# Kernel optimization log

Hardware: AMD Instinct MI355X
Metric: run time of the kernel (lower is better)

Reference implementation:

```python
import jax, jax.numpy as jnp
import numpy as np

H = 1024
V = 50257
L = 4096

def setup_inputs() -> dict:
    key = jax.random.key(0)
    ks = jax.random.split(key, 10)
    s = 1.0 / np.sqrt(H)
    return {
        "input": jax.random.randint(ks[0], (1,), 0, V, dtype=jnp.int64),
        "hidden": jax.random.normal(ks[1], (1, 1, H), dtype=jnp.float32),
        "encoder_hiddens": jax.random.normal(ks[2], (L, H), dtype=jnp.float32),
        "embedding": jax.random.normal(ks[3], (V, H), dtype=jnp.float32),
        "w_ih": jax.random.uniform(ks[4], (3 * H, H), minval=-s, maxval=s, dtype=jnp.float32),
        "w_hh": jax.random.uniform(ks[5], (3 * H, H), minval=-s, maxval=s, dtype=jnp.float32),
        "b_ih": jax.random.uniform(ks[6], (3 * H,), minval=-s, maxval=s, dtype=jnp.float32),
        "b_hh": jax.random.uniform(ks[7], (3 * H,), minval=-s, maxval=s, dtype=jnp.float32),
        "out_w": jax.random.uniform(ks[8], (V, 2 * H), minval=-s, maxval=s, dtype=jnp.float32),
        "out_b": jax.random.uniform(ks[9], (V,), minval=-s, maxval=s, dtype=jnp.float32),
    }


def _gru_step(x, h, w_ih, w_hh, b_ih, b_hh):
    # x, h: (H,). PyTorch GRU cell gate math (gate order: r, z, n).
    gi = w_ih @ x + b_ih                      # (3H,)
    gh = w_hh @ h + b_hh                      # (3H,)
    i_r, i_z, i_n = gi[:H], gi[H:2 * H], gi[2 * H:]
    h_r, h_z, h_n = gh[:H], gh[H:2 * H], gh[2 * H:]
    r = jax.nn.sigmoid(i_r + h_r)
    z = jax.nn.sigmoid(i_z + h_z)
    n = jnp.tanh(i_n + r * h_n)
    return (1.0 - z) * n + z * h


def reference(input, hidden, encoder_hiddens, embedding, w_ih, w_hh, b_ih, b_hh, out_w, out_b):
    # Embedding lookup of single token -> (H,); dropout is identity at inference.
    x = embedding[input].reshape(-1)
    h = hidden[0, 0]                          # (H,)
    h_new = _gru_step(x, h, w_ih, w_hh, b_ih, b_hh)  # (H,)
    # Dot-product attention over encoder hiddens (L, H)
    scores = encoder_hiddens @ h_new          # (L,)
    attn = jax.nn.softmax(scores)             # (L,)
    ctx = attn @ encoder_hiddens              # (H,)
    concat = jnp.concatenate([ctx, h_new])    # (2H,)
    logits = out_w @ concat + out_b           # (V,)
    output = jax.nn.log_softmax(logits)[None, :]  # (1, V)
    return output, h_new[None, None, :]
```

## Files before the change

### kernel.cpp

```cpp
#include <hip/hip_runtime.h>
#include <hip/hip_bf16.h>

#define H 1024
#define V 50257
#define L 4096

__device__ __forceinline__ float sigmoidf_(float x) { return 1.f / (1.f + expf(-x)); }

__device__ __forceinline__ float dot4(float4 w, float4 c) {
    return w.x * c.x + w.y * c.y + w.z * c.z + w.w * c.w;
}

__global__ __launch_bounds__(64) void k_gru(const int* __restrict__ idx,
        const float* __restrict__ hidden, const float* __restrict__ emb,
        const float* __restrict__ w_ih, const float* __restrict__ w_hh,
        const float* __restrict__ b_ih, const float* __restrict__ b_hh,
        float* __restrict__ concat, float* __restrict__ out_h) {
    const int j = blockIdx.x;
    const int lane = threadIdx.x;
    const float* x   = emb + (size_t)idx[0] * H;
    const float* wir = w_ih + (size_t)j * H;
    const float* wiz = wir + (size_t)H * H;
    const float* win = wiz + (size_t)H * H;
    const float* whr = w_hh + (size_t)j * H;
    const float* whz = whr + (size_t)H * H;
    const float* whn = whz + (size_t)H * H;
    float sir = 0, siz = 0, sin_ = 0, shr = 0, shz = 0, shn = 0;
    #pragma unroll
    for (int it = 0; it < 4; ++it) {
        int elem = (it * 64 + lane) * 4;
        float4 xf = *(const float4*)(x + elem);
        float4 hf = *(const float4*)(hidden + elem);
        sir  += dot4(*(const float4*)(wir + elem), xf);
        siz  += dot4(*(const float4*)(wiz + elem), xf);
        sin_ += dot4(*(const float4*)(win + elem), xf);
        shr  += dot4(*(const float4*)(whr + elem), hf);
        shz  += dot4(*(const float4*)(whz + elem), hf);
        shn  += dot4(*(const float4*)(whn + elem), hf);
    }
    #pragma unroll
    for (int off = 32; off; off >>= 1) {
        sir += __shfl_xor(sir, off); siz += __shfl_xor(siz, off);
        sin_ += __shfl_xor(sin_, off); shr += __shfl_xor(shr, off);
        shz += __shfl_xor(shz, off); shn += __shfl_xor(shn, off);
    }
    if (lane == 0) {
        float r = sigmoidf_(sir + b_ih[j]       + shr + b_hh[j]);
        float z = sigmoidf_(siz + b_ih[H + j]   + shz + b_hh[H + j]);
        float n = tanhf(sin_ + b_ih[2*H + j] + r * (shn + b_hh[2*H + j]));
        float hn = (1.f - z) * n + z * hidden[j];
        concat[H + j] = hn;
        out_h[j] = hn;
    }
}

__global__ __launch_bounds__(256) void k_scores(const float* __restrict__ enc,
        const float* __restrict__ concat, float* __restrict__ scores) {
    const int wave = threadIdx.x >> 6, lane = threadIdx.x & 63;
    const int l = blockIdx.x * 4 + wave;
    const float* row = enc + (size_t)l * H;
    const float* h = concat + H;
    float s = 0.f;
    #pragma unroll
    for (int it = 0; it < 4; ++it) {
        int elem = (it * 64 + lane) * 4;
        s += dot4(*(const float4*)(row + elem), *(const float4*)(h + elem));
    }
    #pragma unroll
    for (int off = 32; off; off >>= 1) s += __shfl_xor(s, off);
    if (lane == 0) scores[l] = s;
}

__global__ __launch_bounds__(256) void k_softmax(const float* __restrict__ scores,
                                                 float* __restrict__ attn) {
    __shared__ float sm[8];
    const int t = threadIdx.x, lane = t & 63, wave = t >> 6;
    float v[16];
    float m = -INFINITY;
    #pragma unroll
    for (int i = 0; i < 16; ++i) { v[i] = scores[i * 256 + t]; m = fmaxf(m, v[i]); }
    #pragma unroll
    for (int off = 32; off; off >>= 1) m = fmaxf(m, __shfl_xor(m, off));
    if (lane == 0) sm[wave] = m;
    __syncthreads();
    m = fmaxf(fmaxf(sm[0], sm[1]), fmaxf(sm[2], sm[3]));
    float s = 0.f;
    #pragma unroll
    for (int i = 0; i < 16; ++i) { v[i] = expf(v[i] - m); s += v[i]; }
    #pragma unroll
    for (int off = 32; off; off >>= 1) s += __shfl_xor(s, off);
    __syncthreads();
    if (lane == 0) sm[wave] = s;
    __syncthreads();
    s = sm[0] + sm[1] + sm[2] + sm[3];
    float inv = 1.f / s;
    #pragma unroll
    for (int i = 0; i < 16; ++i) attn[i * 256 + t] = v[i] * inv;
}

__global__ __launch_bounds__(256) void k_ctx_partial(const float* __restrict__ enc,
        const float* __restrict__ attn, float* __restrict__ partial) {
    __shared__ float a[256];
    const int t = threadIdx.x;
    const int r0 = blockIdx.x * 256;
    a[t] = attn[r0 + t];
    __syncthreads();
    float acc0 = 0, acc1 = 0, acc2 = 0, acc3 = 0;
    const float* p = enc + (size_t)r0 * H + t * 4;
    for (int l = 0; l < 256; ++l) {
        float4 w = *(const float4*)p; p += H;
        float al = a[l];
        acc0 += al * w.x; acc1 += al * w.y; acc2 += al * w.z; acc3 += al * w.w;
    }
    *(float4*)(partial + (size_t)blockIdx.x * H + t * 4) = make_float4(acc0, acc1, acc2, acc3);
}

__global__ __launch_bounds__(256) void k_ctx_reduce(const float* __restrict__ partial,
                                                    float* __restrict__ concat) {
    const int c = blockIdx.x * 256 + threadIdx.x;
    float s = 0.f;
    #pragma unroll
    for (int p = 0; p < 16; ++p) s += partial[p * H + c];
    concat[c] = s;
}

__global__ __launch_bounds__(256) void k_logits(const float* __restrict__ out_w,
        const float* __restrict__ out_b, const float* __restrict__ concat,
        float* __restrict__ logits) {
    const int wave = threadIdx.x >> 6, lane = threadIdx.x & 63;
    const int v = blockIdx.x * 4 + wave;
    if (v >= V) return;
    const float* row = out_w + (size_t)v * (2 * H);
    float s = 0.f;
    #pragma unroll
    for (int it = 0; it < 8; ++it) {
        int elem = (it * 64 + lane) * 4;
        s += dot4(*(const float4*)(row + elem), *(const float4*)(concat + elem));
    }
    #pragma unroll
    for (int off = 32; off; off >>= 1) s += __shfl_xor(s, off);
    if (lane == 0) logits[v] = s + out_b[v];
}

__global__ __launch_bounds__(256) void k_lse_partial(const float* __restrict__ logits,
                                                     float* __restrict__ red) {
    __shared__ float sm[4], ss[4];
    const int t = threadIdx.x;
    const int i = blockIdx.x * 256 + t;
    float m = -INFINITY, s = 0.f;
    for (int v = i; v < V; v += 64 * 256) {
        float x = logits[v];
        float M = fmaxf(m, x);
        s = s * expf(m - M) + expf(x - M);
        m = M;
    }
    const int lane = t & 63, wave = t >> 6;
    #pragma unroll
    for (int off = 32; off; off >>= 1) {
        float m2 = __shfl_xor(m, off), s2 = __shfl_xor(s, off);
        float M = fmaxf(m, m2);
        s = s * expf(m - M) + s2 * expf(m2 - M);
        m = M;
    }
    if (lane == 0) { sm[wave] = m; ss[wave] = s; }
    __syncthreads();
    if (t == 0) {
        float M = fmaxf(fmaxf(sm[0], sm[1]), fmaxf(sm[2], sm[3]));
        float S = ss[0] * expf(sm[0] - M) + ss[1] * expf(sm[1] - M) +
                  ss[2] * expf(sm[2] - M) + ss[3] * expf(sm[3] - M);
        red[blockIdx.x] = M;
        red[64 + blockIdx.x] = S;
    }
}

__global__ __launch_bounds__(64) void k_lse_final(const float* __restrict__ red,
                                                  float* __restrict__ C) {
    const int lane = threadIdx.x;
    float m = red[lane], s = red[64 + lane];
    #pragma unroll
    for (int off = 32; off; off >>= 1) {
        float m2 = __shfl_xor(m, off), s2 = __shfl_xor(s, off);
        float M = fmaxf(m, m2);
        s = s * expf(m - M) + s2 * expf(m2 - M);
        m = M;
    }
    if (lane == 0) C[0] = m + logf(s);
}

__global__ __launch_bounds__(256) void k_write(const float* __restrict__ logits,
        const float* __restrict__ C, float* __restrict__ out) {
    const int v = blockIdx.x * 256 + threadIdx.x;
    if (v < V) out[v] = logits[v] - C[0];
}

extern "C" void kernel_launch(void* const* d_in, const int* in_sizes, int n_in,
                              void* d_out, int out_size, void* d_ws, size_t ws_size,
                              hipStream_t stream) {
    const int*   idx    = (const int*)d_in[0];
    const float* hidden = (const float*)d_in[1];
    const float* enc    = (const float*)d_in[2];
    const float* emb    = (const float*)d_in[3];
    const float* w_ih   = (const float*)d_in[4];
    const float* w_hh   = (const float*)d_in[5];
    const float* b_ih   = (const float*)d_in[6];
    const float* b_hh   = (const float*)d_in[7];
    const float* out_w  = (const float*)d_in[8];
    const float* out_b  = (const float*)d_in[9];
    float* out = (float*)d_out;

    float* ws      = (float*)d_ws;
    float* concat  = ws;
    float* scores  = ws + 2048;
    float* attn    = ws + 6144;
    float* partial = ws + 10240;
    float* logits  = ws + 26624;
    float* red     = ws + 76896;
    float* Cv      = ws + 77056;

    k_gru<<<H, 64, 0, stream>>>(idx, hidden, emb, w_ih, w_hh, b_ih, b_hh, concat, out + V);
    k_scores<<<L / 4, 256, 0, stream>>>(enc, concat, scores);
    k_softmax<<<1, 256, 0, stream>>>(scores, attn);
    k_ctx_partial<<<16, 256, 0, stream>>>(enc, attn, partial);
    k_ctx_reduce<<<4, 256, 0, stream>>>(partial, concat);
    k_logits<<<(V + 3) / 4, 256, 0, stream>>>(out_w, out_b, concat, logits);
    k_lse_partial<<<64, 256, 0, stream>>>(logits, red);
    k_lse_final<<<1, 64, 0, stream>>>(red, Cv);
    k_write<<<(V + 255) / 256, 256, 0, stream>>>(logits, Cv, out);
}
```

Baseline: 667.0 us.

## Spread context reduction across more blocks and fuse LSE finalize into write

Splits the attention-weighted context accumulation over 128 blocks instead of 16, with batched unrolled loads to raise memory-level parallelism on the encoder read. The reduction kernel now sums 128 partials per column, and the workspace layout is shifted to fit the larger partial buffer. The final log-sum-exp combine is recomputed inside each block of the write kernel, removing one launch at the cost of redundant per-block work.

```diff
diff --git a/kernel.cpp b/kernel.cpp
--- a/kernel.cpp
+++ b/kernel.cpp
@@ -4,6 +4,8 @@
 #define H 1024
 #define V 50257
 #define L 4096
+#define CTXB 128
+#define ROWS (L / CTXB)
 
 __device__ __forceinline__ float sigmoidf_(float x) { return 1.f / (1.f + expf(-x)); }
 
@@ -100,17 +102,24 @@
 
 __global__ __launch_bounds__(256) void k_ctx_partial(const float* __restrict__ enc,
         const float* __restrict__ attn, float* __restrict__ partial) {
-    __shared__ float a[256];
+    __shared__ float a[ROWS];
     const int t = threadIdx.x;
-    const int r0 = blockIdx.x * 256;
-    a[t] = attn[r0 + t];
+    const int r0 = blockIdx.x * ROWS;
+    if (t < ROWS) a[t] = attn[r0 + t];
     __syncthreads();
     float acc0 = 0, acc1 = 0, acc2 = 0, acc3 = 0;
     const float* p = enc + (size_t)r0 * H + t * 4;
-    for (int l = 0; l < 256; ++l) {
-        float4 w = *(const float4*)p; p += H;
-        float al = a[l];
-        acc0 += al * w.x; acc1 += al * w.y; acc2 += al * w.z; acc3 += al * w.w;
+    #pragma unroll
+    for (int l0 = 0; l0 < ROWS; l0 += 8) {
+        float4 w[8];
+        #pragma unroll
+        for (int k = 0; k < 8; ++k) w[k] = *(const float4*)(p + (size_t)(l0 + k) * H);
+        #pragma unroll
+        for (int k = 0; k < 8; ++k) {
+            float al = a[l0 + k];
+            acc0 += al * w[k].x; acc1 += al * w[k].y;
+            acc2 += al * w[k].z; acc3 += al * w[k].w;
+        }
     }
     *(float4*)(partial + (size_t)blockIdx.x * H + t * 4) = make_float4(acc0, acc1, acc2, acc3);
 }
@@ -119,8 +128,7 @@
                                                     float* __restrict__ concat) {
     const int c = blockIdx.x * 256 + threadIdx.x;
     float s = 0.f;
-    #pragma unroll
-    for (int p = 0; p < 16; ++p) s += partial[p * H + c];
+    for (int p = 0; p < CTXB; ++p) s += partial[(size_t)p * H + c];
     concat[c] = s;
 }
 
@@ -173,24 +181,25 @@
     }
 }
 
-__global__ __launch_bounds__(64) void k_lse_final(const float* __restrict__ red,
-                                                  float* __restrict__ C) {
-    const int lane = threadIdx.x;
-    float m = red[lane], s = red[64 + lane];
-    #pragma unroll
-    for (int off = 32; off; off >>= 1) {
-        float m2 = __shfl_xor(m, off), s2 = __shfl_xor(s, off);
-        float M = fmaxf(m, m2);
-        s = s * expf(m - M) + s2 * expf(m2 - M);
-        m = M;
-    }
-    if (lane == 0) C[0] = m + logf(s);
-}
-
 __global__ __launch_bounds__(256) void k_write(const float* __restrict__ logits,
-        const float* __restrict__ C, float* __restrict__ out) {
-    const int v = blockIdx.x * 256 + threadIdx.x;
-    if (v < V) out[v] = logits[v] - C[0];
+        const float* __restrict__ red, float* __restrict__ out) {
+    __shared__ float sC;
+    const int t = threadIdx.x;
+    if (t < 64) {
+        float m = red[t], s = red[64 + t];
+        #pragma unroll
+        for (int off = 32; off; off >>= 1) {
+            float m2 = __shfl_xor(m, off), s2 = __shfl_xor(s, off);
+            float M = fmaxf(m, m2);
+            s = s * expf(m - M) + s2 * expf(m2 - M);
+            m = M;
+        }
+        if (t == 0) sC = m + logf(s);
+    }
+    __syncthreads();
+    const float C = sC;
+    const int v = blockIdx.x * 256 + t;
+    if (v < V) out[v] = logits[v] - C;
 }
 
 extern "C" void kernel_launch(void* const* d_in, const int* in_sizes, int n_in,
@@ -213,17 +222,15 @@
     float* scores  = ws + 2048;
     float* attn    = ws + 6144;
     float* partial = ws + 10240;
-    float* logits  = ws + 26624;
-    float* red     = ws + 76896;
-    float* Cv      = ws + 77056;
+    float* logits  = ws + 141312;
+    float* red     = ws + 191584;
 
     k_gru<<<H, 64, 0, stream>>>(idx, hidden, emb, w_ih, w_hh, b_ih, b_hh, concat, out + V);
     k_scores<<<L / 4, 256, 0, stream>>>(enc, concat, scores);
     k_softmax<<<1, 256, 0, stream>>>(scores, attn);
-    k_ctx_partial<<<16, 256, 0, stream>>>(enc, attn, partial);
+    k_ctx_partial<<<CTXB, 256, 0, stream>>>(enc, attn, partial);
     k_ctx_reduce<<<4, 256, 0, stream>>>(partial, concat);
     k_logits<<<(V + 3) / 4, 256, 0, stream>>>(out_w, out_b, concat, logits);
     k_lse_partial<<<64, 256, 0, stream>>>(logits, red);
-    k_lse_final<<<1, 64, 0, stream>>>(red, Cv);
-    k_write<<<(V + 255) / 256, 256, 0, stream>>>(logits, Cv, out);
-}
+    k_write<<<(V + 255) / 256, 256, 0, stream>>>(logits, red, out);
+}
```

New measurement: 657.9 us. No clear change (-1.4%).
